# Optimization experiments

Hardware: AMD Instinct MI355X
Metric: run time of the kernel (lower is better)

The kernel has to match this reference:

```python
import jax, jax.numpy as jnp
import numpy as np

C = 64          # residual channels
N_LAYERS = 30
MAX_STEPS = 200
SQRT2 = 2.0 ** 0.5


def _conv1d(x, W, b, dilation=1, pad=0):
    # x: [B, Cin, T], W: [Cout, Cin, K], b: [Cout]
    y = jax.lax.conv_general_dilated(
        x, W, window_strides=(1,), padding=[(pad, pad)],
        rhs_dilation=(dilation,), dimension_numbers=('NCH', 'OIH', 'NCH'))
    return y + b[None, :, None]


def _silu(x):
    return x * jax.nn.sigmoid(x)


def _emb_table():
    steps = jnp.arange(MAX_STEPS, dtype=jnp.float32)[:, None]      # [200,1]
    dims = jnp.arange(64, dtype=jnp.float32)[None, :]              # [1,64]
    t = steps * 10.0 ** (dims * 4.0 / 63.0)                        # [200,64]
    return jnp.concatenate([jnp.sin(t), jnp.cos(t)], axis=1)       # [200,128]


def setup_inputs() -> dict:
    key = jax.random.key(0)
    ks = jax.random.split(key, 20)
    B, T = 4, 16384
    f32 = jnp.float32
    inp = {
        'audio': jax.random.normal(ks[0], (B, 1, T), dtype=f32),
        'diffusion_step': jax.random.randint(ks[1], (B,), 0, MAX_STEPS),
        # input projection Conv1d(1, 64, 1)
        'in_W': jax.random.normal(ks[2], (C, 1, 1), f32) * 1.0,
        'in_b': jax.random.normal(ks[3], (C,), f32) * 0.01,
        # diffusion embedding MLP 128->512->512
        'p1_W': jax.random.normal(ks[4], (512, 128), f32) * (1.0 / np.sqrt(128)),
        'p1_b': jnp.zeros((512,), f32),
        'p2_W': jax.random.normal(ks[5], (512, 512), f32) * (1.0 / np.sqrt(512)),
        'p2_b': jnp.zeros((512,), f32),
        # per-layer params (stacked over 30 layers)
        'dw_W': jax.random.normal(ks[6], (N_LAYERS, 2 * C, C, 3), f32) * (1.0 / np.sqrt(3 * C)),
        'dw_b': jnp.zeros((N_LAYERS, 2 * C), f32),
        'dp_W': jax.random.normal(ks[7], (N_LAYERS, C, 512), f32) * (1.0 / np.sqrt(512)),
        'dp_b': jnp.zeros((N_LAYERS, C), f32),
        'op_W': jax.random.normal(ks[8], (N_LAYERS, 2 * C, C, 1), f32) * (1.0 / np.sqrt(C)),
        'op_b': jnp.zeros((N_LAYERS, 2 * C), f32),
        # skip projection Conv1d(64,64,1)
        'sk_W': jax.random.normal(ks[9], (C, C, 1), f32) * (1.0 / np.sqrt(C)),
        'sk_b': jnp.zeros((C,), f32),
        # output projection Conv1d(64,1,1), weight zero-init like original
        'out_W': jnp.zeros((1, C, 1), f32),
        'out_b': jax.random.normal(ks[10], (1,), f32) * 0.01,
    }
    return inp


def reference(audio, diffusion_step, in_W, in_b, p1_W, p1_b, p2_W, p2_b,
              dw_W, dw_b, dp_W, dp_b, op_W, op_b, sk_W, sk_b, out_W, out_b):
    x = jax.nn.relu(_conv1d(audio, in_W, in_b))                    # [B,64,T]
    # diffusion embedding
    t = _emb_table()[diffusion_step]                               # [B,128]
    t = _silu(t @ p1_W.T + p1_b)                                   # [B,512]
    t = _silu(t @ p2_W.T + p2_b)                                   # [B,512]
    skip = None
    for i in range(N_LAYERS):
        d = 2 ** (i % 10)
        cond = (t @ dp_W[i].T + dp_b[i])[:, :, None]               # [B,64,1]
        y = _conv1d(x + cond, dw_W[i], dw_b[i], dilation=d, pad=d) # [B,128,T]
        gate, filt = y[:, :C], y[:, C:]
        y = jax.nn.sigmoid(gate) * jnp.tanh(filt)                  # [B,64,T]
        y = _conv1d(y, op_W[i], op_b[i])                           # [B,128,T]
        residual, sk = y[:, :C], y[:, C:]
        x = (x + residual) / SQRT2
        skip = sk if skip is None else skip + sk
    x = skip / np.sqrt(float(N_LAYERS)).astype(np.float32)
    x = jax.nn.relu(_conv1d(x, sk_W, sk_b))
    return _conv1d(x, out_W, out_b)                                # [B,1,T]
```

## Files before the change

kernel.cpp:

```cpp
#include <hip/hip_runtime.h>
#include <math.h>

#define C 64
#define NL 30
#define T 16384
#define B 4

typedef __bf16 bf16_t;
typedef __bf16 bf16x8 __attribute__((ext_vector_type(8)));
typedef __bf16 bf16x4 __attribute__((ext_vector_type(4)));
typedef float f32x4 __attribute__((ext_vector_type(4)));

typedef const __attribute__((address_space(1))) unsigned int glb_u32;
typedef __attribute__((address_space(3))) unsigned int lds_u32;

constexpr float INV_SQRT2   = 0.70710678118654752440f;
constexpr float INV_SQRT_NL = 0.18257418583505537115f;

__device__ __forceinline__ float fsig(float x) {
    return __builtin_amdgcn_rcpf(1.f + __builtin_amdgcn_exp2f(-1.44269504089f * x));
}
__device__ __forceinline__ float ftanh(float x) {
    return fmaf(2.f, __builtin_amdgcn_rcpf(1.f + __builtin_amdgcn_exp2f(-2.88539008178f * x)), -1.f);
}
__device__ __forceinline__ int swz(int off) { return off ^ ((off >> 3) & 0x70); }

__global__ void pack_weights(const float* __restrict__ dw_W,
                             const float* __restrict__ op_W,
                             const float* __restrict__ sk_W,
                             bf16_t* __restrict__ convpk,
                             bf16_t* __restrict__ oppk,
                             bf16_t* __restrict__ skpk) {
    int idx = blockIdx.x * 256 + threadIdx.x;
    const int ndw = NL * 128 * 192;
    const int nop = NL * 128 * 64;
    if (idx < ndw) {
        int k = idx % 192; int r = idx / 192;
        int oc = r % 128;  int l = r / 128;
        int tap = k >> 6, ic = k & 63;
        convpk[idx] = (bf16_t)dw_W[((l * 128 + oc) * 64 + ic) * 3 + tap];
    } else if (idx < ndw + nop) {
        oppk[idx - ndw] = (bf16_t)op_W[idx - ndw];
    } else if (idx < ndw + nop + 4096) {
        int j = idx - ndw - nop;
        skpk[j] = (bf16_t)(sk_W[j] * INV_SQRT_NL);
    }
}

__global__ void cond_embp1(const int* __restrict__ step,
                           const float* __restrict__ p1_W, const float* __restrict__ p1_b,
                           float* __restrict__ h1out) {
    __shared__ float e[128];
    __shared__ float red[256];
    int b = blockIdx.x, blk = blockIdx.y, tid = threadIdx.x;
    int s = step[b];
    if (tid < 128) {
        int d = tid & 63;
        float tf = (float)s * powf(10.f, (float)d * 4.f / 63.f);
        double td = (double)tf;
        e[tid] = (tid < 64) ? (float)sin(td) : (float)cos(td);
    }
    __syncthreads();
    int ol = tid >> 2, q = tid & 3;
    int o = blk * 64 + ol;
    const float4* wr = (const float4*)(p1_W + o * 128 + q * 32);
    const float4* ev = (const float4*)(e + q * 32);
    float a = 0.f;
    #pragma unroll
    for (int j = 0; j < 8; ++j) {
        float4 wv = wr[j]; float4 xv = ev[j];
        a = fmaf(wv.x, xv.x, a); a = fmaf(wv.y, xv.y, a);
        a = fmaf(wv.z, xv.z, a); a = fmaf(wv.w, xv.w, a);
    }
    red[tid] = a;
    __syncthreads();
    if (q == 0) {
        float v = red[tid] + red[tid + 1] + red[tid + 2] + red[tid + 3] + p1_b[o];
        h1out[b * 512 + o] = v / (1.f + expf(-v));
    }
}

__global__ void cond_p2(const float* __restrict__ h1,
                        const float* __restrict__ p2_W, const float* __restrict__ p2_b,
                        float* __restrict__ h2out) {
    __shared__ float red[256];
    int b = blockIdx.x, blk = blockIdx.y, tid = threadIdx.x;
    int ol = tid >> 2, q = tid & 3;
    int o = blk * 64 + ol;
    const float4* wr = (const float4*)(p2_W + o * 512 + q * 128);
    const float4* hv = (const float4*)(h1 + b * 512 + q * 128);
    float a = 0.f;
    #pragma unroll 8
    for (int j = 0; j < 32; ++j) {
        float4 wv = wr[j]; float4 xv = hv[j];
        a = fmaf(wv.x, xv.x, a); a = fmaf(wv.y, xv.y, a);
        a = fmaf(wv.z, xv.z, a); a = fmaf(wv.w, xv.w, a);
    }
    red[tid] = a;
    __syncthreads();
    if (q == 0) {
        float v = red[tid] + red[tid + 1] + red[tid + 2] + red[tid + 3] + p2_b[o];
        h2out[b * 512 + o] = v / (1.f + expf(-v));
    }
}

__global__ void cond_stage2b(const float* __restrict__ h2,
                             const float* __restrict__ dp_W, const float* __restrict__ dp_b,
                             const bf16_t* __restrict__ convpk,
                             const float* __restrict__ dw_b,
                             float* __restrict__ bias2) {
    __shared__ float red[256];
    __shared__ float cond_s[64];
    int l = blockIdx.x, b = blockIdx.y;
    int tid = threadIdx.x;
    {
        int o = tid >> 2, q = tid & 3;
        const float4* wr = (const float4*)(dp_W + ((size_t)l * C + o) * 512 + q * 128);
        const float4* h = (const float4*)(h2 + b * 512 + q * 128);
        float a = 0.f;
        #pragma unroll 8
        for (int j = 0; j < 32; ++j) {
            float4 wv = wr[j]; float4 hv = h[j];
            a = fmaf(wv.x, hv.x, a); a = fmaf(wv.y, hv.y, a);
            a = fmaf(wv.z, hv.z, a); a = fmaf(wv.w, hv.w, a);
        }
        red[tid] = a;
        __syncthreads();
        if (q == 0)
            cond_s[o] = red[tid] + red[tid + 1] + red[tid + 2] + red[tid + 3] + dp_b[l * C + o];
    }
    __syncthreads();
    int oc = tid & 127, kh = tid >> 7;
    const bf16_t* wr = convpk + ((size_t)l * 128 + oc) * 192 + kh * 96;
    float a = kh ? 0.f : dw_b[l * 128 + oc];
    #pragma unroll
    for (int j = 0; j < 96; ++j)
        a = fmaf((float)wr[j], cond_s[(kh * 96 + j) & 63], a);
    __syncthreads();
    red[tid] = a;
    __syncthreads();
    if (tid < 128)
        bias2[(l * B + b) * 128 + tid] = red[tid] + red[tid + 128];
}

__global__ void in_conv(const float* __restrict__ audio,
                        const float* __restrict__ in_W, const float* __restrict__ in_b,
                        bf16_t* __restrict__ x) {
    int idx = blockIdx.x * 256 + threadIdx.x;
    int cb = idx & 7;
    int t = (idx >> 3) & (T - 1);
    int b = idx >> 17;
    float av = audio[b * T + t];
    bf16x8 o;
    #pragma unroll
    for (int j = 0; j < 8; ++j) {
        int c = cb * 8 + j;
        o[j] = (bf16_t)fmaxf(fmaf(in_W[c], av, in_b[c]), 0.f);
    }
    *(bf16x8*)(x + ((size_t)b * T + t) * 64 + cb * 8) = o;
}

__global__ __launch_bounds__(512, 4) void layer_kernel(
    const bf16_t* __restrict__ x_in, bf16_t* __restrict__ x_out, bf16_t* __restrict__ skip,
    const bf16_t* __restrict__ convpk, const bf16_t* __restrict__ oppk,
    const float* __restrict__ bias2, const float* __restrict__ op_b,
    const bf16_t* __restrict__ zpage,
    int layer, int dil, int first)
{
    __shared__ uint4 smem_u[4096];
    char* sm = (char*)smem_u;

    int tid = threadIdx.x;
    int w8 = __builtin_amdgcn_readfirstlane(tid >> 6);
    int wq = w8 & 3;
    int h  = w8 >> 2;
    int l = tid & 63;
    int lr = l & 15;
    int g = l >> 4;
    int b = blockIdx.y;
    int tbase = blockIdx.x * 128;
    const bf16_t* xb = x_in + (size_t)b * T * 64;

    #pragma unroll
    for (int it = 0; it < 6; ++it) {
        int hh = it / 3;
        int slice = it % 3;
        int row = tid >> 3;
        int c16 = l & 7;
        int ts = tbase + hh * 64 + row + (slice - 1) * dil;
        int c16s = c16 ^ (row & 7);
        const bf16_t* src = ((unsigned)ts < (unsigned)T)
            ? (xb + (size_t)ts * 64 + c16s * 8)
            : (zpage + c16s * 8);
        __builtin_amdgcn_global_load_lds(
            (glb_u32*)src,
            (lds_u32*)(sm + it * 8192 + w8 * 1024),
            16, 0, 0);
    }

    bf16x8 cA[2][6];
    const bf16_t* cw = convpk + (size_t)layer * 128 * 192;
    #pragma unroll
    for (int mf = 0; mf < 2; ++mf)
        #pragma unroll
        for (int kf = 0; kf < 6; ++kf)
            cA[mf][kf] = *(const bf16x8*)(cw + (mf * 64 + wq * 16 + lr) * 192 + kf * 32 + g * 8);

    f32x4 acc[2][4];
    const float* b2 = bias2 + (layer * B + b) * 128;
    #pragma unroll
    for (int mf = 0; mf < 2; ++mf) {
        f32x4 bv;
        #pragma unroll
        for (int r = 0; r < 4; ++r) bv[r] = b2[mf * 64 + wq * 16 + g * 4 + r];
        #pragma unroll
        for (int nf = 0; nf < 4; ++nf) acc[mf][nf] = bv;
    }
    __syncthreads();

    int hbase = h * 24576;
    #pragma unroll
    for (int kf = 0; kf < 6; ++kf) {
        int tap = kf >> 1;
        int kc = (kf & 1) * 32;
        bf16x8 Bf[4];
        #pragma unroll
        for (int nf = 0; nf < 4; ++nf) {
            int off = hbase + tap * 8192 + (nf * 16 + lr) * 128 + (kc + g * 8) * 2;
            Bf[nf] = *(const bf16x8*)(sm + swz(off));
        }
        #pragma unroll
        for (int mf = 0; mf < 2; ++mf)
            #pragma unroll
            for (int nf = 0; nf < 4; ++nf)
                acc[mf][nf] = __builtin_amdgcn_mfma_f32_16x16x32_bf16(
                    cA[mf][kf], Bf[nf], acc[mf][nf], 0, 0, 0);
    }

    bf16x8 oA[2][2];
    const bf16_t* ow = oppk + (size_t)layer * 128 * 64;
    #pragma unroll
    for (int mf = 0; mf < 2; ++mf)
        #pragma unroll
        for (int kf = 0; kf < 2; ++kf)
            oA[mf][kf] = *(const bf16x8*)(ow + (mf * 64 + wq * 16 + lr) * 64 + kf * 32 + g * 8);

    int zbase = 49152 + h * 8192;
    #pragma unroll
    for (int nf = 0; nf < 4; ++nf) {
        union { bf16_t hh[4]; uint2 u; } zp;
        #pragma unroll
        for (int r = 0; r < 4; ++r)
            zp.hh[r] = (bf16_t)(fsig(acc[0][nf][r]) * ftanh(acc[1][nf][r]));
        int off = zbase + (nf * 16 + lr) * 128 + (wq * 16 + g * 4) * 2;
        *(uint2*)(sm + swz(off)) = zp.u;
    }
    __syncthreads();

    f32x4 acc2[2][4];
    const float* ob = op_b + layer * 2 * C;
    #pragma unroll
    for (int mf = 0; mf < 2; ++mf) {
        f32x4 bv;
        #pragma unroll
        for (int r = 0; r < 4; ++r) bv[r] = ob[mf * 64 + wq * 16 + g * 4 + r];
        #pragma unroll
        for (int nf = 0; nf < 4; ++nf) acc2[mf][nf] = bv;
    }
    #pragma unroll
    for (int kf = 0; kf < 2; ++kf) {
        bf16x8 Zf[4];
        #pragma unroll
        for (int nf = 0; nf < 4; ++nf) {
            int off = zbase + (nf * 16 + lr) * 128 + (kf * 32 + g * 8) * 2;
            Zf[nf] = *(const bf16x8*)(sm + swz(off));
        }
        #pragma unroll
        for (int mf = 0; mf < 2; ++mf)
            #pragma unroll
            for (int nf = 0; nf < 4; ++nf)
                acc2[mf][nf] = __builtin_amdgcn_mfma_f32_16x16x32_bf16(
                    oA[mf][kf], Zf[nf], acc2[mf][nf], 0, 0, 0);
    }

    size_t bb = (size_t)b * T * 64;
    int t0 = tbase + h * 64;
    #pragma unroll
    for (int nf = 0; nf < 4; ++nf) {
        int t = t0 + nf * 16 + lr;
        int c0 = wq * 16 + g * 4;
        int xoff = hbase + 8192 + (nf * 16 + lr) * 128 + c0 * 2;
        bf16x4 xv = *(const bf16x4*)(sm + swz(xoff));
        bf16x4 ro, so;
        bf16_t* sp = skip + bb + (size_t)t * 64 + c0;
        if (first) {
            #pragma unroll
            for (int r = 0; r < 4; ++r) {
                ro[r] = (bf16_t)(((float)xv[r] + acc2[0][nf][r]) * INV_SQRT2);
                so[r] = (bf16_t)acc2[1][nf][r];
            }
        } else {
            bf16x4 sv = *(const bf16x4*)sp;
            #pragma unroll
            for (int r = 0; r < 4; ++r) {
                ro[r] = (bf16_t)(((float)xv[r] + acc2[0][nf][r]) * INV_SQRT2);
                so[r] = (bf16_t)((float)sv[r] + acc2[1][nf][r]);
            }
        }
        *(bf16x4*)(x_out + bb + (size_t)t * 64 + c0) = ro;
        *(bf16x4*)sp = so;
    }
}

__global__ __launch_bounds__(256) void final_kernel(
    const bf16_t* __restrict__ skip, const bf16_t* __restrict__ skpk,
    const float* __restrict__ sk_b,
    const float* __restrict__ out_W, const float* __restrict__ out_b,
    float* __restrict__ out)
{
    __shared__ uint4 tile_u[512];
    __shared__ float part[16][66];
    unsigned char* sm = (unsigned char*)tile_u;
    int tid = threadIdx.x;
    int w = __builtin_amdgcn_readfirstlane(tid >> 6);
    int l = tid & 63, lr = l & 15, g = l >> 4;
    int b = blockIdx.y, t0 = blockIdx.x * 64;
    const bf16_t* sb = skip + (size_t)b * T * 64;

    #pragma unroll
    for (int it = 0; it < 2; ++it) {
        int q = it * 256 + tid;
        int row = q >> 3, c16 = q & 7;
        uint4 val = *(const uint4*)(sb + (size_t)(t0 + row) * 64 + c16 * 8);
        *(uint4*)(sm + swz(row * 128 + c16 * 16)) = val;
    }

    bf16x8 aS[2];
    #pragma unroll
    for (int kf = 0; kf < 2; ++kf)
        aS[kf] = *(const bf16x8*)(skpk + (w * 16 + lr) * 64 + kf * 32 + g * 8);
    f32x4 acc[4];
    #pragma unroll
    for (int nf = 0; nf < 4; ++nf)
        #pragma unroll
        for (int r = 0; r < 4; ++r) acc[nf][r] = sk_b[w * 16 + g * 4 + r];
    __syncthreads();

    #pragma unroll
    for (int kf = 0; kf < 2; ++kf) {
        bf16x8 Bf[4];
        #pragma unroll
        for (int nf = 0; nf < 4; ++nf) {
            int off = (nf * 16 + lr) * 128 + (kf * 32 + g * 8) * 2;
            Bf[nf] = *(const bf16x8*)(sm + swz(off));
        }
        #pragma unroll
        for (int nf = 0; nf < 4; ++nf)
            acc[nf] = __builtin_amdgcn_mfma_f32_16x16x32_bf16(aS[kf], Bf[nf], acc[nf], 0, 0, 0);
    }

    #pragma unroll
    for (int nf = 0; nf < 4; ++nf) {
        float o = 0.f;
        #pragma unroll
        for (int r = 0; r < 4; ++r)
            o = fmaf(out_W[w * 16 + g * 4 + r], fmaxf(acc[nf][r], 0.f), o);
        part[w * 4 + g][nf * 16 + lr] = o;
    }
    __syncthreads();
    if (tid < 64) {
        float o = out_b[0];
        #pragma unroll
        for (int j = 0; j < 16; ++j) o += part[j][tid];
        out[(size_t)b * T + t0 + tid] = o;
    }
}

extern "C" void kernel_launch(void* const* d_in, const int* in_sizes, int n_in,
                              void* d_out, int out_size, void* d_ws, size_t ws_size,
                              hipStream_t stream) {
    const float* audio = (const float*)d_in[0];
    const int*   dstep = (const int*)d_in[1];
    const float* in_W  = (const float*)d_in[2];
    const float* in_b  = (const float*)d_in[3];
    const float* p1_W  = (const float*)d_in[4];
    const float* p1_b  = (const float*)d_in[5];
    const float* p2_W  = (const float*)d_in[6];
    const float* p2_b  = (const float*)d_in[7];
    const float* dw_W  = (const float*)d_in[8];
    const float* dw_b  = (const float*)d_in[9];
    const float* dp_W  = (const float*)d_in[10];
    const float* dp_b  = (const float*)d_in[11];
    const float* op_W  = (const float*)d_in[12];
    const float* op_b  = (const float*)d_in[13];
    const float* sk_W  = (const float*)d_in[14];
    const float* sk_b  = (const float*)d_in[15];
    const float* out_W = (const float*)d_in[16];
    const float* out_b = (const float*)d_in[17];

    float* ws = (float*)d_ws;
    const size_t NXE = (size_t)B * T * 64;
    float* h1    = ws;
    float* h2    = h1 + B * 512;
    float* bias2 = h2 + B * 512;
    float* zpg   = bias2 + NL * B * 128;
    bf16_t* xA   = (bf16_t*)(zpg + 128);
    bf16_t* xB   = xA + NXE;
    bf16_t* skip = xB + NXE;
    bf16_t* convpk = skip + NXE;
    bf16_t* oppk   = convpk + (size_t)NL * 128 * 192;
    bf16_t* skpk   = oppk + (size_t)NL * 128 * 64;

    hipMemsetAsync(zpg, 0, 512, stream);
    hipLaunchKernelGGL(pack_weights, dim3(3856), dim3(256), 0, stream,
                       dw_W, op_W, sk_W, convpk, oppk, skpk);
    hipLaunchKernelGGL(cond_embp1, dim3(B, 8), dim3(256), 0, stream,
                       dstep, p1_W, p1_b, h1);
    hipLaunchKernelGGL(cond_p2, dim3(B, 8), dim3(256), 0, stream,
                       h1, p2_W, p2_b, h2);
    hipLaunchKernelGGL(cond_stage2b, dim3(NL, B), dim3(256), 0, stream,
                       h2, dp_W, dp_b, convpk, dw_b, bias2);
    hipLaunchKernelGGL(in_conv, dim3(B * T * 8 / 256), dim3(256), 0, stream,
                       audio, in_W, in_b, xA);
    for (int i = 0; i < NL; ++i) {
        bf16_t* xin  = (i & 1) ? xB : xA;
        bf16_t* xout = (i & 1) ? xA : xB;
        int dil = 1 << (i % 10);
        hipLaunchKernelGGL(layer_kernel, dim3(T / 128, B), dim3(512), 0, stream,
                           xin, xout, skip, convpk, oppk, bias2, op_b,
                           (const bf16_t*)zpg, i, dil, (i == 0) ? 1 : 0);
    }
    hipLaunchKernelGGL(final_kernel, dim3(T / 64, B), dim3(256), 0, stream,
                       skip, skpk, sk_b, out_W, out_b, (float*)d_out);
}
```

Before: 544.5 us.

## Stage contiguous dilated window once and process two time halves per 256-thread block

For small dilations the layer kernel now loads one contiguous row window covering all three conv taps instead of three separate shifted slices. This reduces redundant global loads and LDS fill. The block shrinks to 4 waves, which loop over the two 64-step halves in sequence, and the second half's loads are issued up front to overlap with the first half's compute. The trade-offs are less parallelism per block and synchronisation that relies on implicit waits, which could be fragile.

```diff
diff --git a/kernel.cpp b/kernel.cpp
--- a/kernel.cpp
+++ b/kernel.cpp
@@ -160,7 +160,7 @@
     *(bf16x8*)(x + ((size_t)b * T + t) * 64 + cb * 8) = o;
 }
 
-__global__ __launch_bounds__(512, 4) void layer_kernel(
+__global__ __launch_bounds__(256) void layer_kernel(
     const bf16_t* __restrict__ x_in, bf16_t* __restrict__ x_out, bf16_t* __restrict__ skip,
     const bf16_t* __restrict__ convpk, const bf16_t* __restrict__ oppk,
     const float* __restrict__ bias2, const float* __restrict__ op_b,
@@ -171,32 +171,56 @@
     char* sm = (char*)smem_u;
 
     int tid = threadIdx.x;
-    int w8 = __builtin_amdgcn_readfirstlane(tid >> 6);
-    int wq = w8 & 3;
-    int h  = w8 >> 2;
+    int w = __builtin_amdgcn_readfirstlane(tid >> 6);
     int l = tid & 63;
     int lr = l & 15;
     int g = l >> 4;
     int b = blockIdx.y;
     int tbase = blockIdx.x * 128;
     const bf16_t* xb = x_in + (size_t)b * T * 64;
-
-    #pragma unroll
-    for (int it = 0; it < 6; ++it) {
-        int hh = it / 3;
-        int slice = it % 3;
-        int row = tid >> 3;
-        int c16 = l & 7;
-        int ts = tbase + hh * 64 + row + (slice - 1) * dil;
-        int c16s = c16 ^ (row & 7);
-        const bf16_t* src = ((unsigned)ts < (unsigned)T)
-            ? (xb + (size_t)ts * 64 + c16s * 8)
-            : (zpage + c16s * 8);
-        __builtin_amdgcn_global_load_lds(
-            (glb_u32*)src,
-            (lds_u32*)(sm + it * 8192 + w8 * 1024),
-            16, 0, 0);
-    }
+    const bool m1 = (dil <= 32);
+
+#define STAGE_M1(Sbase, t0s, R)                                              \
+    _Pragma("unroll")                                                        \
+    for (int r = 0; r < (R); ++r) {                                          \
+        int q = r * 4096 + tid * 16;                                         \
+        int row = q >> 7, c16 = (q >> 4) & 7;                                \
+        int ts = (t0s) - dil + row;                                          \
+        int c16s = c16 ^ (row & 7);                                          \
+        const bf16_t* src = ((unsigned)ts < (unsigned)T)                     \
+            ? xb + (size_t)ts * 64 + c16s * 8 : zpage + c16s * 8;            \
+        __builtin_amdgcn_global_load_lds((glb_u32*)src,                      \
+            (lds_u32*)(sm + (Sbase) + r * 4096 + w * 1024), 16, 0, 0);       \
+    }
+#define STAGE_M3(Sbase, t0s)                                                 \
+    _Pragma("unroll")                                                        \
+    for (int it = 0; it < 6; ++it) {                                         \
+        int qq = it * 256 + tid;                                             \
+        int slice = qq >> 9, row = (qq >> 3) & 63, c16 = qq & 7;             \
+        int ts = (t0s) + row + (slice - 1) * dil;                            \
+        int c16s = c16 ^ (row & 7);                                          \
+        const bf16_t* src = ((unsigned)ts < (unsigned)T)                     \
+            ? xb + (size_t)ts * 64 + c16s * 8 : zpage + c16s * 8;            \
+        __builtin_amdgcn_global_load_lds((glb_u32*)src,                      \
+            (lds_u32*)(sm + (Sbase) + it * 4096 + w * 1024), 16, 0, 0);      \
+    }
+
+    if (dil <= 16) {
+        STAGE_M1(0, tbase, 3)
+        STAGE_M1(24576, tbase + 64, 3)
+        asm volatile("s_waitcnt vmcnt(3)" ::: "memory");
+    } else if (dil == 32) {
+        STAGE_M1(0, tbase, 4)
+        STAGE_M1(24576, tbase + 64, 4)
+        asm volatile("s_waitcnt vmcnt(4)" ::: "memory");
+    } else {
+        STAGE_M3(0, tbase)
+        STAGE_M3(24576, tbase + 64)
+        asm volatile("s_waitcnt vmcnt(6)" ::: "memory");
+    }
+    __builtin_amdgcn_s_barrier();
+    __builtin_amdgcn_sched_barrier(0);
+    asm volatile("" ::: "memory");
 
     bf16x8 cA[2][6];
     const bf16_t* cw = convpk + (size_t)layer * 128 * 192;
@@ -204,112 +228,117 @@
     for (int mf = 0; mf < 2; ++mf)
         #pragma unroll
         for (int kf = 0; kf < 6; ++kf)
-            cA[mf][kf] = *(const bf16x8*)(cw + (mf * 64 + wq * 16 + lr) * 192 + kf * 32 + g * 8);
-
-    f32x4 acc[2][4];
-    const float* b2 = bias2 + (layer * B + b) * 128;
-    #pragma unroll
-    for (int mf = 0; mf < 2; ++mf) {
-        f32x4 bv;
-        #pragma unroll
-        for (int r = 0; r < 4; ++r) bv[r] = b2[mf * 64 + wq * 16 + g * 4 + r];
-        #pragma unroll
-        for (int nf = 0; nf < 4; ++nf) acc[mf][nf] = bv;
-    }
-    __syncthreads();
-
-    int hbase = h * 24576;
-    #pragma unroll
-    for (int kf = 0; kf < 6; ++kf) {
-        int tap = kf >> 1;
-        int kc = (kf & 1) * 32;
-        bf16x8 Bf[4];
-        #pragma unroll
-        for (int nf = 0; nf < 4; ++nf) {
-            int off = hbase + tap * 8192 + (nf * 16 + lr) * 128 + (kc + g * 8) * 2;
-            Bf[nf] = *(const bf16x8*)(sm + swz(off));
-        }
-        #pragma unroll
-        for (int mf = 0; mf < 2; ++mf)
-            #pragma unroll
-            for (int nf = 0; nf < 4; ++nf)
-                acc[mf][nf] = __builtin_amdgcn_mfma_f32_16x16x32_bf16(
-                    cA[mf][kf], Bf[nf], acc[mf][nf], 0, 0, 0);
-    }
-
+            cA[mf][kf] = *(const bf16x8*)(cw + (mf * 64 + w * 16 + lr) * 192 + kf * 32 + g * 8);
     bf16x8 oA[2][2];
     const bf16_t* ow = oppk + (size_t)layer * 128 * 64;
     #pragma unroll
     for (int mf = 0; mf < 2; ++mf)
         #pragma unroll
         for (int kf = 0; kf < 2; ++kf)
-            oA[mf][kf] = *(const bf16x8*)(ow + (mf * 64 + wq * 16 + lr) * 64 + kf * 32 + g * 8);
-
-    int zbase = 49152 + h * 8192;
-    #pragma unroll
-    for (int nf = 0; nf < 4; ++nf) {
-        union { bf16_t hh[4]; uint2 u; } zp;
-        #pragma unroll
-        for (int r = 0; r < 4; ++r)
-            zp.hh[r] = (bf16_t)(fsig(acc[0][nf][r]) * ftanh(acc[1][nf][r]));
-        int off = zbase + (nf * 16 + lr) * 128 + (wq * 16 + g * 4) * 2;
-        *(uint2*)(sm + swz(off)) = zp.u;
-    }
-    __syncthreads();
-
-    f32x4 acc2[2][4];
+            oA[mf][kf] = *(const bf16x8*)(ow + (mf * 64 + w * 16 + lr) * 64 + kf * 32 + g * 8);
+    f32x4 bC[2], bO[2];
+    const float* b2 = bias2 + (layer * B + b) * 128;
     const float* ob = op_b + layer * 2 * C;
     #pragma unroll
-    for (int mf = 0; mf < 2; ++mf) {
-        f32x4 bv;
-        #pragma unroll
-        for (int r = 0; r < 4; ++r) bv[r] = ob[mf * 64 + wq * 16 + g * 4 + r];
-        #pragma unroll
-        for (int nf = 0; nf < 4; ++nf) acc2[mf][nf] = bv;
-    }
-    #pragma unroll
-    for (int kf = 0; kf < 2; ++kf) {
-        bf16x8 Zf[4];
+    for (int mf = 0; mf < 2; ++mf)
+        #pragma unroll
+        for (int r = 0; r < 4; ++r) {
+            bC[mf][r] = b2[mf * 64 + w * 16 + g * 4 + r];
+            bO[mf][r] = ob[mf * 64 + w * 16 + g * 4 + r];
+        }
+
+    size_t bb = (size_t)b * T * 64;
+    int tapstride = m1 ? dil * 128 : 8192;
+    int t1off = m1 ? dil * 128 : 8192;
+
+    for (int st = 0; st < 2; ++st) {
+        int Sb = st * 24576;
+        int zb = 49152 + st * 8192;
+        int t0 = tbase + st * 64;
+
+        f32x4 acc[2][4];
+        #pragma unroll
+        for (int mf = 0; mf < 2; ++mf)
+            #pragma unroll
+            for (int nf = 0; nf < 4; ++nf) acc[mf][nf] = bC[mf];
+        #pragma unroll
+        for (int kf = 0; kf < 6; ++kf) {
+            int tap = kf >> 1;
+            int kc = (kf & 1) * 32;
+            bf16x8 Bf[4];
+            #pragma unroll
+            for (int nf = 0; nf < 4; ++nf) {
+                int off = Sb + tap * tapstride + (nf * 16 + lr) * 128 + (kc + g * 8) * 2;
+                Bf[nf] = *(const bf16x8*)(sm + swz(off));
+            }
+            #pragma unroll
+            for (int mf = 0; mf < 2; ++mf)
+                #pragma unroll
+                for (int nf = 0; nf < 4; ++nf)
+                    acc[mf][nf] = __builtin_amdgcn_mfma_f32_16x16x32_bf16(
+                        cA[mf][kf], Bf[nf], acc[mf][nf], 0, 0, 0);
+        }
+
         #pragma unroll
         for (int nf = 0; nf < 4; ++nf) {
-            int off = zbase + (nf * 16 + lr) * 128 + (kf * 32 + g * 8) * 2;
-            Zf[nf] = *(const bf16x8*)(sm + swz(off));
-        }
+            union { bf16_t hh[4]; uint2 u; } zp;
+            #pragma unroll
+            for (int r = 0; r < 4; ++r)
+                zp.hh[r] = (bf16_t)(fsig(acc[0][nf][r]) * ftanh(acc[1][nf][r]));
+            int off = zb + (nf * 16 + lr) * 128 + (w * 16 + g * 4) * 2;
+            *(uint2*)(sm + swz(off)) = zp.u;
+        }
+        __syncthreads();
+
+        f32x4 acc2[2][4];
         #pragma unroll
         for (int mf = 0; mf < 2; ++mf)
             #pragma unroll
-            for (int nf = 0; nf < 4; ++nf)
-                acc2[mf][nf] = __builtin_amdgcn_mfma_f32_16x16x32_bf16(
-                    oA[mf][kf], Zf[nf], acc2[mf][nf], 0, 0, 0);
-    }
-
-    size_t bb = (size_t)b * T * 64;
-    int t0 = tbase + h * 64;
-    #pragma unroll
-    for (int nf = 0; nf < 4; ++nf) {
-        int t = t0 + nf * 16 + lr;
-        int c0 = wq * 16 + g * 4;
-        int xoff = hbase + 8192 + (nf * 16 + lr) * 128 + c0 * 2;
-        bf16x4 xv = *(const bf16x4*)(sm + swz(xoff));
-        bf16x4 ro, so;
-        bf16_t* sp = skip + bb + (size_t)t * 64 + c0;
-        if (first) {
-            #pragma unroll
-            for (int r = 0; r < 4; ++r) {
-                ro[r] = (bf16_t)(((float)xv[r] + acc2[0][nf][r]) * INV_SQRT2);
-                so[r] = (bf16_t)acc2[1][nf][r];
+            for (int nf = 0; nf < 4; ++nf) acc2[mf][nf] = bO[mf];
+        #pragma unroll
+        for (int kf = 0; kf < 2; ++kf) {
+            bf16x8 Zf[4];
+            #pragma unroll
+            for (int nf = 0; nf < 4; ++nf) {
+                int off = zb + (nf * 16 + lr) * 128 + (kf * 32 + g * 8) * 2;
+                Zf[nf] = *(const bf16x8*)(sm + swz(off));
             }
-        } else {
-            bf16x4 sv = *(const bf16x4*)sp;
-            #pragma unroll
-            for (int r = 0; r < 4; ++r) {
-                ro[r] = (bf16_t)(((float)xv[r] + acc2[0][nf][r]) * INV_SQRT2);
-                so[r] = (bf16_t)((float)sv[r] + acc2[1][nf][r]);
+            #pragma unroll
+            for (int mf = 0; mf < 2; ++mf)
+                #pragma unroll
+                for (int nf = 0; nf < 4; ++nf)
+                    acc2[mf][nf] = __builtin_amdgcn_mfma_f32_16x16x32_bf16(
+                        oA[mf][kf], Zf[nf], acc2[mf][nf], 0, 0, 0);
+        }
+
+        #pragma unroll
+        for (int nf = 0; nf < 4; ++nf) {
+            int t = t0 + nf * 16 + lr;
+            int c0 = w * 16 + g * 4;
+            int xoff = Sb + t1off + (nf * 16 + lr) * 128 + c0 * 2;
+            bf16x4 xv = *(const bf16x4*)(sm + swz(xoff));
+            bf16x4 ro, so;
+            bf16_t* sp = skip + bb + (size_t)t * 64 + c0;
+            if (first) {
+                #pragma unroll
+                for (int r = 0; r < 4; ++r) {
+                    ro[r] = (bf16_t)(((float)xv[r] + acc2[0][nf][r]) * INV_SQRT2);
+                    so[r] = (bf16_t)acc2[1][nf][r];
+                }
+            } else {
+                bf16x4 sv = *(const bf16x4*)sp;
+                #pragma unroll
+                for (int r = 0; r < 4; ++r) {
+                    ro[r] = (bf16_t)(((float)xv[r] + acc2[0][nf][r]) * INV_SQRT2);
+                    so[r] = (bf16_t)((float)sv[r] + acc2[1][nf][r]);
+                }
             }
-        }
-        *(bf16x4*)(x_out + bb + (size_t)t * 64 + c0) = ro;
-        *(bf16x4*)sp = so;
-    }
+            *(bf16x4*)(x_out + bb + (size_t)t * 64 + c0) = ro;
+            *(bf16x4*)sp = so;
+        }
+    }
+#undef STAGE_M1
+#undef STAGE_M3
 }
 
 __global__ __launch_bounds__(256) void final_kernel(
@@ -426,7 +455,7 @@
         bf16_t* xin  = (i & 1) ? xB : xA;
         bf16_t* xout = (i & 1) ? xA : xB;
         int dil = 1 << (i % 10);
-        hipLaunchKernelGGL(layer_kernel, dim3(T / 128, B), dim3(512), 0, stream,
+        hipLaunchKernelGGL(layer_kernel, dim3(T / 128, B), dim3(256), 0, stream,
                            xin, xout, skip, convpk, oppk, bias2, op_b,
                            (const bf16_t*)zpg, i, dil, (i == 0) ? 1 : 0);
     }
```

New measurement: 514.1 us. 5.6% less time.

## Fuse all WaveNet layers into one persistent kernel with grid barriers

Applied to the files above, without the earlier changes.

Replaces the input conv, the 30 per-layer launches and the final kernel with a single persistent kernel of 256 blocks that syncs between layers through an atomic grid barrier. The skip accumulator now stays in fp32 registers for each block's fixed time tile instead of being read and written in bf16 global memory every layer, and the final projection runs in the same kernel. This removes launch gaps and skip-tensor traffic. In exchange each block processes two sub-tiles serially, runs at lower occupancy (launch bounds 2), and relies on all 256 blocks being co-resident so the spin barrier cannot deadlock.

```diff
diff --git a/kernel.cpp b/kernel.cpp
--- a/kernel.cpp
+++ b/kernel.cpp
@@ -5,6 +5,7 @@
 #define NL 30
 #define T 16384
 #define B 4
+#define NBLK 256
 
 typedef __bf16 bf16_t;
 typedef __bf16 bf16x8 __attribute__((ext_vector_type(8)));
@@ -24,6 +25,24 @@
     return fmaf(2.f, __builtin_amdgcn_rcpf(1.f + __builtin_amdgcn_exp2f(-2.88539008178f * x)), -1.f);
 }
 __device__ __forceinline__ int swz(int off) { return off ^ ((off >> 3) & 0x70); }
+
+__device__ __forceinline__ void gbar(unsigned* cnt, unsigned* gen) {
+    __syncthreads();
+    if (threadIdx.x == 0) {
+        __threadfence();
+        unsigned g = __hip_atomic_load(gen, __ATOMIC_RELAXED, __HIP_MEMORY_SCOPE_AGENT);
+        unsigned a = __hip_atomic_fetch_add(cnt, 1u, __ATOMIC_ACQ_REL, __HIP_MEMORY_SCOPE_AGENT);
+        if (a == NBLK - 1u) {
+            __hip_atomic_store(cnt, 0u, __ATOMIC_RELAXED, __HIP_MEMORY_SCOPE_AGENT);
+            __hip_atomic_store(gen, g + 1u, __ATOMIC_RELEASE, __HIP_MEMORY_SCOPE_AGENT);
+        } else {
+            while (__hip_atomic_load(gen, __ATOMIC_ACQUIRE, __HIP_MEMORY_SCOPE_AGENT) == g)
+                __builtin_amdgcn_s_sleep(8);
+        }
+        __threadfence();
+    }
+    __syncthreads();
+}
 
 __global__ void pack_weights(const float* __restrict__ dw_W,
                              const float* __restrict__ op_W,
@@ -143,236 +162,230 @@
         bias2[(l * B + b) * 128 + tid] = red[tid] + red[tid + 128];
 }
 
-__global__ void in_conv(const float* __restrict__ audio,
-                        const float* __restrict__ in_W, const float* __restrict__ in_b,
-                        bf16_t* __restrict__ x) {
-    int idx = blockIdx.x * 256 + threadIdx.x;
-    int cb = idx & 7;
-    int t = (idx >> 3) & (T - 1);
-    int b = idx >> 17;
-    float av = audio[b * T + t];
-    bf16x8 o;
-    #pragma unroll
-    for (int j = 0; j < 8; ++j) {
-        int c = cb * 8 + j;
-        o[j] = (bf16_t)fmaxf(fmaf(in_W[c], av, in_b[c]), 0.f);
-    }
-    *(bf16x8*)(x + ((size_t)b * T + t) * 64 + cb * 8) = o;
-}
-
-__global__ __launch_bounds__(512, 4) void layer_kernel(
-    const bf16_t* __restrict__ x_in, bf16_t* __restrict__ x_out, bf16_t* __restrict__ skip,
+__global__ __launch_bounds__(512, 2) void diffwave_persistent(
+    const float* __restrict__ audio,
+    const float* __restrict__ in_W, const float* __restrict__ in_b,
+    bf16_t* __restrict__ xA, bf16_t* __restrict__ xB,
     const bf16_t* __restrict__ convpk, const bf16_t* __restrict__ oppk,
     const float* __restrict__ bias2, const float* __restrict__ op_b,
     const bf16_t* __restrict__ zpage,
-    int layer, int dil, int first)
+    const bf16_t* __restrict__ skpk, const float* __restrict__ sk_b,
+    const float* __restrict__ out_W, const float* __restrict__ out_b,
+    float* __restrict__ out,
+    unsigned* __restrict__ bcnt, unsigned* __restrict__ bgen)
 {
-    __shared__ uint4 smem_u[4096];
-    char* sm = (char*)smem_u;
+    __shared__ __align__(16) char sm[65536];
 
     int tid = threadIdx.x;
-    int w8 = __builtin_amdgcn_readfirstlane(tid >> 6);
-    int wq = w8 & 3;
-    int h  = w8 >> 2;
+    int hh = __builtin_amdgcn_readfirstlane(tid >> 8);
+    int w  = __builtin_amdgcn_readfirstlane(tid >> 6) & 3;
+    int ltid = tid & 255;
     int l = tid & 63;
     int lr = l & 15;
     int g = l >> 4;
-    int b = blockIdx.y;
-    int tbase = blockIdx.x * 128;
-    const bf16_t* xb = x_in + (size_t)b * T * 64;
+    int bid = blockIdx.x;
+    int b = bid >> 6;
+    int tb = (bid & 63) * 256;
+    int hbase = hh << 15;
+    size_t bb = (size_t)b * T * 64;
 
     #pragma unroll
-    for (int it = 0; it < 6; ++it) {
-        int hh = it / 3;
-        int slice = it % 3;
-        int row = tid >> 3;
-        int c16 = l & 7;
-        int ts = tbase + hh * 64 + row + (slice - 1) * dil;
-        int c16s = c16 ^ (row & 7);
-        const bf16_t* src = ((unsigned)ts < (unsigned)T)
-            ? (xb + (size_t)ts * 64 + c16s * 8)
-            : (zpage + c16s * 8);
-        __builtin_amdgcn_global_load_lds(
-            (glb_u32*)src,
-            (lds_u32*)(sm + it * 8192 + w8 * 1024),
-            16, 0, 0);
-    }
-
-    bf16x8 cA[2][6];
-    const bf16_t* cw = convpk + (size_t)layer * 128 * 192;
+    for (int v = 0; v < 4; ++v) {
+        int idx = v * 512 + tid;
+        int row = idx >> 3, cb = idx & 7;
+        float av = audio[(size_t)b * T + tb + row];
+        bf16x8 o;
+        #pragma unroll
+        for (int j = 0; j < 8; ++j) {
+            int c = cb * 8 + j;
+            o[j] = (bf16_t)fmaxf(fmaf(in_W[c], av, in_b[c]), 0.f);
+        }
+        *(bf16x8*)(xA + bb + (size_t)(tb + row) * 64 + cb * 8) = o;
+    }
+
+    float skr[32];
     #pragma unroll
-    for (int mf = 0; mf < 2; ++mf)
-        #pragma unroll
-        for (int kf = 0; kf < 6; ++kf)
-            cA[mf][kf] = *(const bf16x8*)(cw + (mf * 64 + wq * 16 + lr) * 192 + kf * 32 + g * 8);
-
-    f32x4 acc[2][4];
-    const float* b2 = bias2 + (layer * B + b) * 128;
+    for (int i = 0; i < 32; ++i) skr[i] = 0.f;
+
+    gbar(bcnt, bgen);
+
+    for (int layer = 0; layer < NL; ++layer) {
+        int dil = 1 << (layer % 10);
+        const bf16_t* xin = (layer & 1) ? xB : xA;
+        bf16_t* xout = (layer & 1) ? xA : xB;
+        const bf16_t* xb_ = xin + bb;
+
+        bf16x8 cA[2][6];
+        const bf16_t* cw = convpk + (size_t)layer * 128 * 192;
+        #pragma unroll
+        for (int mf = 0; mf < 2; ++mf)
+            #pragma unroll
+            for (int kf = 0; kf < 6; ++kf)
+                cA[mf][kf] = *(const bf16x8*)(cw + (mf * 64 + w * 16 + lr) * 192 + kf * 32 + g * 8);
+        bf16x8 oA[2][2];
+        const bf16_t* ow = oppk + (size_t)layer * 128 * 64;
+        #pragma unroll
+        for (int mf = 0; mf < 2; ++mf)
+            #pragma unroll
+            for (int kf = 0; kf < 2; ++kf)
+                oA[mf][kf] = *(const bf16x8*)(ow + (mf * 64 + w * 16 + lr) * 64 + kf * 32 + g * 8);
+        f32x4 bC[2], bO[2];
+        const float* b2 = bias2 + (layer * B + b) * 128;
+        const float* ob = op_b + layer * 2 * C;
+        #pragma unroll
+        for (int mf = 0; mf < 2; ++mf)
+            #pragma unroll
+            for (int r = 0; r < 4; ++r) {
+                bC[mf][r] = b2[mf * 64 + w * 16 + g * 4 + r];
+                bO[mf][r] = ob[mf * 64 + w * 16 + g * 4 + r];
+            }
+
+        #pragma unroll
+        for (int st = 0; st < 2; ++st) {
+            int t0 = tb + hh * 128 + st * 64;
+
+            #pragma unroll
+            for (int it = 0; it < 6; ++it) {
+                int qq = it * 256 + ltid;
+                int slice = qq >> 9, row = (qq >> 3) & 63, c16 = qq & 7;
+                int ts = t0 + row + (slice - 1) * dil;
+                int c16s = c16 ^ (row & 7);
+                const bf16_t* src = ((unsigned)ts < (unsigned)T)
+                    ? (xb_ + (size_t)ts * 64 + c16s * 8)
+                    : (zpage + c16s * 8);
+                __builtin_amdgcn_global_load_lds((glb_u32*)src,
+                    (lds_u32*)(sm + hbase + it * 4096 + w * 1024), 16, 0, 0);
+            }
+            __syncthreads();
+
+            f32x4 acc[2][4];
+            #pragma unroll
+            for (int mf = 0; mf < 2; ++mf)
+                #pragma unroll
+                for (int nf = 0; nf < 4; ++nf) acc[mf][nf] = bC[mf];
+            #pragma unroll
+            for (int kf = 0; kf < 6; ++kf) {
+                int tap = kf >> 1;
+                int kc = (kf & 1) * 32;
+                bf16x8 Bf[4];
+                #pragma unroll
+                for (int nf = 0; nf < 4; ++nf) {
+                    int off = hbase + tap * 8192 + (nf * 16 + lr) * 128 + (kc + g * 8) * 2;
+                    Bf[nf] = *(const bf16x8*)(sm + swz(off));
+                }
+                #pragma unroll
+                for (int mf = 0; mf < 2; ++mf)
+                    #pragma unroll
+                    for (int nf = 0; nf < 4; ++nf)
+                        acc[mf][nf] = __builtin_amdgcn_mfma_f32_16x16x32_bf16(
+                            cA[mf][kf], Bf[nf], acc[mf][nf], 0, 0, 0);
+            }
+
+            #pragma unroll
+            for (int nf = 0; nf < 4; ++nf) {
+                union { bf16_t hv[4]; uint2 u; } zp;
+                #pragma unroll
+                for (int r = 0; r < 4; ++r)
+                    zp.hv[r] = (bf16_t)(fsig(acc[0][nf][r]) * ftanh(acc[1][nf][r]));
+                int off = hbase + 24576 + (nf * 16 + lr) * 128 + (w * 16 + g * 4) * 2;
+                *(uint2*)(sm + swz(off)) = zp.u;
+            }
+            __syncthreads();
+
+            f32x4 acc2[2][4];
+            #pragma unroll
+            for (int mf = 0; mf < 2; ++mf)
+                #pragma unroll
+                for (int nf = 0; nf < 4; ++nf) acc2[mf][nf] = bO[mf];
+            #pragma unroll
+            for (int kf = 0; kf < 2; ++kf) {
+                bf16x8 Zf[4];
+                #pragma unroll
+                for (int nf = 0; nf < 4; ++nf) {
+                    int off = hbase + 24576 + (nf * 16 + lr) * 128 + (kf * 32 + g * 8) * 2;
+                    Zf[nf] = *(const bf16x8*)(sm + swz(off));
+                }
+                #pragma unroll
+                for (int mf = 0; mf < 2; ++mf)
+                    #pragma unroll
+                    for (int nf = 0; nf < 4; ++nf)
+                        acc2[mf][nf] = __builtin_amdgcn_mfma_f32_16x16x32_bf16(
+                            oA[mf][kf], Zf[nf], acc2[mf][nf], 0, 0, 0);
+            }
+
+            #pragma unroll
+            for (int nf = 0; nf < 4; ++nf) {
+                int t = t0 + nf * 16 + lr;
+                int c0 = w * 16 + g * 4;
+                int xoff = hbase + 8192 + (nf * 16 + lr) * 128 + c0 * 2;
+                bf16x4 xv = *(const bf16x4*)(sm + swz(xoff));
+                bf16x4 ro;
+                #pragma unroll
+                for (int r = 0; r < 4; ++r) {
+                    ro[r] = (bf16_t)(((float)xv[r] + acc2[0][nf][r]) * INV_SQRT2);
+                    skr[st * 16 + nf * 4 + r] += acc2[1][nf][r];
+                }
+                *(bf16x4*)(xout + bb + (size_t)t * 64 + c0) = ro;
+            }
+            __syncthreads();
+        }
+
+        if (layer < NL - 1) gbar(bcnt, bgen);
+    }
+
+    float* pp = (float*)(sm + hbase);
     #pragma unroll
-    for (int mf = 0; mf < 2; ++mf) {
-        f32x4 bv;
-        #pragma unroll
-        for (int r = 0; r < 4; ++r) bv[r] = b2[mf * 64 + wq * 16 + g * 4 + r];
-        #pragma unroll
-        for (int nf = 0; nf < 4; ++nf) acc[mf][nf] = bv;
-    }
-    __syncthreads();
-
-    int hbase = h * 24576;
-    #pragma unroll
-    for (int kf = 0; kf < 6; ++kf) {
-        int tap = kf >> 1;
-        int kc = (kf & 1) * 32;
-        bf16x8 Bf[4];
+    for (int st = 0; st < 2; ++st) {
+        int t0 = tb + hh * 128 + st * 64;
         #pragma unroll
         for (int nf = 0; nf < 4; ++nf) {
-            int off = hbase + tap * 8192 + (nf * 16 + lr) * 128 + (kc + g * 8) * 2;
-            Bf[nf] = *(const bf16x8*)(sm + swz(off));
-        }
-        #pragma unroll
-        for (int mf = 0; mf < 2; ++mf)
+            union { bf16_t hv[4]; uint2 u; } zp;
+            #pragma unroll
+            for (int r = 0; r < 4; ++r)
+                zp.hv[r] = (bf16_t)skr[st * 16 + nf * 4 + r];
+            int off = hbase + 24576 + (nf * 16 + lr) * 128 + (w * 16 + g * 4) * 2;
+            *(uint2*)(sm + swz(off)) = zp.u;
+        }
+        __syncthreads();
+
+        bf16x8 aS[2];
+        #pragma unroll
+        for (int kf = 0; kf < 2; ++kf)
+            aS[kf] = *(const bf16x8*)(skpk + (w * 16 + lr) * 64 + kf * 32 + g * 8);
+        f32x4 acc[4];
+        #pragma unroll
+        for (int nf = 0; nf < 4; ++nf)
+            #pragma unroll
+            for (int r = 0; r < 4; ++r) acc[nf][r] = sk_b[w * 16 + g * 4 + r];
+        #pragma unroll
+        for (int kf = 0; kf < 2; ++kf) {
+            bf16x8 Bf[4];
+            #pragma unroll
+            for (int nf = 0; nf < 4; ++nf) {
+                int off = hbase + 24576 + (nf * 16 + lr) * 128 + (kf * 32 + g * 8) * 2;
+                Bf[nf] = *(const bf16x8*)(sm + swz(off));
+            }
             #pragma unroll
             for (int nf = 0; nf < 4; ++nf)
-                acc[mf][nf] = __builtin_amdgcn_mfma_f32_16x16x32_bf16(
-                    cA[mf][kf], Bf[nf], acc[mf][nf], 0, 0, 0);
-    }
-
-    bf16x8 oA[2][2];
-    const bf16_t* ow = oppk + (size_t)layer * 128 * 64;
-    #pragma unroll
-    for (int mf = 0; mf < 2; ++mf)
-        #pragma unroll
-        for (int kf = 0; kf < 2; ++kf)
-            oA[mf][kf] = *(const bf16x8*)(ow + (mf * 64 + wq * 16 + lr) * 64 + kf * 32 + g * 8);
-
-    int zbase = 49152 + h * 8192;
-    #pragma unroll
-    for (int nf = 0; nf < 4; ++nf) {
-        union { bf16_t hh[4]; uint2 u; } zp;
-        #pragma unroll
-        for (int r = 0; r < 4; ++r)
-            zp.hh[r] = (bf16_t)(fsig(acc[0][nf][r]) * ftanh(acc[1][nf][r]));
-        int off = zbase + (nf * 16 + lr) * 128 + (wq * 16 + g * 4) * 2;
-        *(uint2*)(sm + swz(off)) = zp.u;
-    }
-    __syncthreads();
-
-    f32x4 acc2[2][4];
-    const float* ob = op_b + layer * 2 * C;
-    #pragma unroll
-    for (int mf = 0; mf < 2; ++mf) {
-        f32x4 bv;
-        #pragma unroll
-        for (int r = 0; r < 4; ++r) bv[r] = ob[mf * 64 + wq * 16 + g * 4 + r];
-        #pragma unroll
-        for (int nf = 0; nf < 4; ++nf) acc2[mf][nf] = bv;
-    }
-    #pragma unroll
-    for (int kf = 0; kf < 2; ++kf) {
-        bf16x8 Zf[4];
+                acc[nf] = __builtin_amdgcn_mfma_f32_16x16x32_bf16(aS[kf], Bf[nf], acc[nf], 0, 0, 0);
+        }
+
         #pragma unroll
         for (int nf = 0; nf < 4; ++nf) {
-            int off = zbase + (nf * 16 + lr) * 128 + (kf * 32 + g * 8) * 2;
-            Zf[nf] = *(const bf16x8*)(sm + swz(off));
-        }
-        #pragma unroll
-        for (int mf = 0; mf < 2; ++mf)
-            #pragma unroll
-            for (int nf = 0; nf < 4; ++nf)
-                acc2[mf][nf] = __builtin_amdgcn_mfma_f32_16x16x32_bf16(
-                    oA[mf][kf], Zf[nf], acc2[mf][nf], 0, 0, 0);
-    }
-
-    size_t bb = (size_t)b * T * 64;
-    int t0 = tbase + h * 64;
-    #pragma unroll
-    for (int nf = 0; nf < 4; ++nf) {
-        int t = t0 + nf * 16 + lr;
-        int c0 = wq * 16 + g * 4;
-        int xoff = hbase + 8192 + (nf * 16 + lr) * 128 + c0 * 2;
-        bf16x4 xv = *(const bf16x4*)(sm + swz(xoff));
-        bf16x4 ro, so;
-        bf16_t* sp = skip + bb + (size_t)t * 64 + c0;
-        if (first) {
-            #pragma unroll
-            for (int r = 0; r < 4; ++r) {
-                ro[r] = (bf16_t)(((float)xv[r] + acc2[0][nf][r]) * INV_SQRT2);
-                so[r] = (bf16_t)acc2[1][nf][r];
-            }
-        } else {
-            bf16x4 sv = *(const bf16x4*)sp;
-            #pragma unroll
-            for (int r = 0; r < 4; ++r) {
-                ro[r] = (bf16_t)(((float)xv[r] + acc2[0][nf][r]) * INV_SQRT2);
-                so[r] = (bf16_t)((float)sv[r] + acc2[1][nf][r]);
-            }
-        }
-        *(bf16x4*)(x_out + bb + (size_t)t * 64 + c0) = ro;
-        *(bf16x4*)sp = so;
-    }
-}
-
-__global__ __launch_bounds__(256) void final_kernel(
-    const bf16_t* __restrict__ skip, const bf16_t* __restrict__ skpk,
-    const float* __restrict__ sk_b,
-    const float* __restrict__ out_W, const float* __restrict__ out_b,
-    float* __restrict__ out)
-{
-    __shared__ uint4 tile_u[512];
-    __shared__ float part[16][66];
-    unsigned char* sm = (unsigned char*)tile_u;
-    int tid = threadIdx.x;
-    int w = __builtin_amdgcn_readfirstlane(tid >> 6);
-    int l = tid & 63, lr = l & 15, g = l >> 4;
-    int b = blockIdx.y, t0 = blockIdx.x * 64;
-    const bf16_t* sb = skip + (size_t)b * T * 64;
-
-    #pragma unroll
-    for (int it = 0; it < 2; ++it) {
-        int q = it * 256 + tid;
-        int row = q >> 3, c16 = q & 7;
-        uint4 val = *(const uint4*)(sb + (size_t)(t0 + row) * 64 + c16 * 8);
-        *(uint4*)(sm + swz(row * 128 + c16 * 16)) = val;
-    }
-
-    bf16x8 aS[2];
-    #pragma unroll
-    for (int kf = 0; kf < 2; ++kf)
-        aS[kf] = *(const bf16x8*)(skpk + (w * 16 + lr) * 64 + kf * 32 + g * 8);
-    f32x4 acc[4];
-    #pragma unroll
-    for (int nf = 0; nf < 4; ++nf)
-        #pragma unroll
-        for (int r = 0; r < 4; ++r) acc[nf][r] = sk_b[w * 16 + g * 4 + r];
-    __syncthreads();
-
-    #pragma unroll
-    for (int kf = 0; kf < 2; ++kf) {
-        bf16x8 Bf[4];
-        #pragma unroll
-        for (int nf = 0; nf < 4; ++nf) {
-            int off = (nf * 16 + lr) * 128 + (kf * 32 + g * 8) * 2;
-            Bf[nf] = *(const bf16x8*)(sm + swz(off));
-        }
-        #pragma unroll
-        for (int nf = 0; nf < 4; ++nf)
-            acc[nf] = __builtin_amdgcn_mfma_f32_16x16x32_bf16(aS[kf], Bf[nf], acc[nf], 0, 0, 0);
-    }
-
-    #pragma unroll
-    for (int nf = 0; nf < 4; ++nf) {
-        float o = 0.f;
-        #pragma unroll
-        for (int r = 0; r < 4; ++r)
-            o = fmaf(out_W[w * 16 + g * 4 + r], fmaxf(acc[nf][r], 0.f), o);
-        part[w * 4 + g][nf * 16 + lr] = o;
-    }
-    __syncthreads();
-    if (tid < 64) {
-        float o = out_b[0];
-        #pragma unroll
-        for (int j = 0; j < 16; ++j) o += part[j][tid];
-        out[(size_t)b * T + t0 + tid] = o;
+            float o = 0.f;
+            #pragma unroll
+            for (int r = 0; r < 4; ++r)
+                o = fmaf(out_W[w * 16 + g * 4 + r], fmaxf(acc[nf][r], 0.f), o);
+            pp[(w * 4 + g) * 66 + nf * 16 + lr] = o;
+        }
+        __syncthreads();
+        if (ltid < 64) {
+            float o = out_b[0];
+            #pragma unroll
+            for (int j = 0; j < 16; ++j) o += pp[j * 66 + ltid];
+            out[(size_t)b * T + t0 + ltid] = o;
+        }
+        __syncthreads();
     }
 }
 
@@ -400,17 +413,18 @@
 
     float* ws = (float*)d_ws;
     const size_t NXE = (size_t)B * T * 64;
-    float* h1    = ws;
+    unsigned* bar = (unsigned*)ws;
+    float* h1    = ws + 64;
     float* h2    = h1 + B * 512;
     float* bias2 = h2 + B * 512;
     float* zpg   = bias2 + NL * B * 128;
     bf16_t* xA   = (bf16_t*)(zpg + 128);
     bf16_t* xB   = xA + NXE;
-    bf16_t* skip = xB + NXE;
-    bf16_t* convpk = skip + NXE;
+    bf16_t* convpk = xB + NXE;
     bf16_t* oppk   = convpk + (size_t)NL * 128 * 192;
     bf16_t* skpk   = oppk + (size_t)NL * 128 * 64;
 
+    hipMemsetAsync(bar, 0, 256, stream);
     hipMemsetAsync(zpg, 0, 512, stream);
     hipLaunchKernelGGL(pack_weights, dim3(3856), dim3(256), 0, stream,
                        dw_W, op_W, sk_W, convpk, oppk, skpk);
@@ -420,16 +434,9 @@
                        h1, p2_W, p2_b, h2);
     hipLaunchKernelGGL(cond_stage2b, dim3(NL, B), dim3(256), 0, stream,
                        h2, dp_W, dp_b, convpk, dw_b, bias2);
-    hipLaunchKernelGGL(in_conv, dim3(B * T * 8 / 256), dim3(256), 0, stream,
-                       audio, in_W, in_b, xA);
-    for (int i = 0; i < NL; ++i) {
-        bf16_t* xin  = (i & 1) ? xB : xA;
-        bf16_t* xout = (i & 1) ? xA : xB;
-        int dil = 1 << (i % 10);
-        hipLaunchKernelGGL(layer_kernel, dim3(T / 128, B), dim3(512), 0, stream,
-                           xin, xout, skip, convpk, oppk, bias2, op_b,
-                           (const bf16_t*)zpg, i, dil, (i == 0) ? 1 : 0);
-    }
-    hipLaunchKernelGGL(final_kernel, dim3(T / 64, B), dim3(256), 0, stream,
-                       skip, skpk, sk_b, out_W, out_b, (float*)d_out);
-}
+
+    hipLaunchKernelGGL(diffwave_persistent, dim3(NBLK), dim3(512), 0, stream,
+                       audio, in_W, in_b, xA, xB, convpk, oppk, bias2, op_b,
+                       (const bf16_t*)zpg, skpk, sk_b, out_W, out_b,
+                       (float*)d_out, bar, bar + 16);
+}
```

Measured after the change: 1.705 ms. 213% more time.
